# Performance work log

Measured on AMD Instinct MI355X. Metric: run time of the kernel, lower is better.

Reference implementation:

```python
import jax, jax.numpy as jnp
import numpy as np

EMBED_DIM = 1024
NUM_HEADS = 16
HEAD_DIM = EMBED_DIM // NUM_HEADS
BATCH = 2
SEQ = 2048


def setup_inputs() -> dict:
    key = jax.random.key(0)
    ks = jax.random.split(key, 7)
    bound = 1.0 / np.sqrt(EMBED_DIM)  # nn.Linear default init range
    x = jax.random.normal(ks[0], (BATCH, SEQ, EMBED_DIM), dtype=jnp.float32)
    attn_mask = jnp.ones((BATCH, SEQ), dtype=jnp.int32)
    Wq = jax.random.uniform(ks[1], (EMBED_DIM, EMBED_DIM), jnp.float32, -bound, bound)
    bq = jax.random.uniform(ks[2], (EMBED_DIM,), jnp.float32, -bound, bound)
    Wk = jax.random.uniform(ks[3], (EMBED_DIM, EMBED_DIM), jnp.float32, -bound, bound)
    bk = jax.random.uniform(ks[4], (EMBED_DIM,), jnp.float32, -bound, bound)
    Wv = jax.random.uniform(ks[5], (EMBED_DIM, EMBED_DIM), jnp.float32, -bound, bound)
    bv = jax.random.uniform(ks[6], (EMBED_DIM,), jnp.float32, -bound, bound)
    return {"x": x, "attn_mask": attn_mask, "inv_scale": 8,
            "Wq": Wq, "bq": bq, "Wk": Wk, "bk": bk, "Wv": Wv, "bv": bv}


def reference(x, attn_mask, inv_scale, Wq, bq, Wk, bk, Wv, bv):
    bs, seq_len, _ = x.shape
    # Linear layers (torch: y = x @ W.T + b; here W stored as [in,out])
    def split_heads(y):
        return y.reshape(bs, seq_len, NUM_HEADS, HEAD_DIM).transpose(0, 2, 1, 3)  # [b,h,s,d]
    q = split_heads(x @ Wq + bq)
    k = split_heads(x @ Wk + bk)
    v = split_heads(x @ Wv + bv)
    scores = jnp.einsum('bhqd,bhkd->bhqk', q, k) / jnp.asarray(inv_scale, x.dtype)
    mask = (attn_mask == 0)[:, None, None, :]  # True where masked
    scores = jnp.where(mask, -jnp.inf, scores)
    attn = jax.nn.softmax(scores, axis=-1)
    out = jnp.einsum('bhqk,bhkd->bhqd', attn, v)  # [b,h,s,d]
    return out
```

## Files before the change

### kernel.cpp

```cpp
#include <hip/hip_runtime.h>
#include <stdint.h>

typedef __bf16 bf16x8 __attribute__((ext_vector_type(8)));
typedef float f32x4 __attribute__((ext_vector_type(4)));
typedef uint32_t u32x2 __attribute__((ext_vector_type(2)));
typedef uint32_t u32x4 __attribute__((ext_vector_type(4)));

#define MFMA16(a, b, c) __builtin_amdgcn_mfma_f32_16x16x32_bf16((a), (b), (c), 0, 0, 0)

#if __has_builtin(__builtin_amdgcn_exp2f)
#define EXP2F(x) __builtin_amdgcn_exp2f(x)
#else
#define EXP2F(x) exp2f(x)
#endif

__device__ __forceinline__ void gload16(const void* gsrc, void* ldst) {
  __builtin_amdgcn_global_load_lds((__attribute__((address_space(1))) void*)gsrc,
                                   (__attribute__((address_space(3))) void*)ldst, 16, 0, 0);
}

__device__ __forceinline__ uint32_t pkbf(float a, float b) {
  uint16_t ua = __builtin_bit_cast(uint16_t, (__bf16)a);
  uint16_t ub = __builtin_bit_cast(uint16_t, (__bf16)b);
  return (uint32_t)ua | ((uint32_t)ub << 16);
}

__global__ __launch_bounds__(256) void prep_kernel(
    const float* __restrict__ x, const float* __restrict__ Wq,
    const float* __restrict__ Wk, const float* __restrict__ Wv,
    ushort* __restrict__ xb, ushort* __restrict__ wt) {
  int tid = blockIdx.x * 256 + threadIdx.x;
  if (tid < 524288) {
    const f32x4* xp = (const f32x4*)x;
    f32x4 a = xp[tid * 2], b = xp[tid * 2 + 1];
    u32x4 o;
    o[0] = pkbf(a[0], a[1]);
    o[1] = pkbf(a[2], a[3]);
    o[2] = pkbf(b[0], b[1]);
    o[3] = pkbf(b[2], b[3]);
    *(u32x4*)(xb + (size_t)tid * 8) = o;
  } else {
    int r = tid - 524288;
    int mtx = r >> 17;
    int q = r & 131071;
    int n = q & 1023, kc = q >> 10;
    const float* W = (mtx == 0) ? Wq : (mtx == 1) ? Wk : Wv;
    const float* src = W + (size_t)kc * 8 * 1024 + n;
    float v0 = src[0], v1 = src[1024], v2 = src[2048], v3 = src[3072];
    float v4 = src[4096], v5 = src[5120], v6 = src[6144], v7 = src[7168];
    u32x4 o;
    o[0] = pkbf(v0, v1);
    o[1] = pkbf(v2, v3);
    o[2] = pkbf(v4, v5);
    o[3] = pkbf(v6, v7);
    *(u32x4*)(wt + (size_t)mtx * 1048576 + (size_t)n * 1024 + kc * 8) = o;
  }
}

__global__ __launch_bounds__(256, 2) void gemm_qkv(
    const ushort* __restrict__ xb, const ushort* __restrict__ wt,
    const float* __restrict__ bq, const float* __restrict__ bk,
    const float* __restrict__ bv, ushort* __restrict__ Qb,
    ushort* __restrict__ Kb, ushort* __restrict__ Vt) {
  __shared__ ushort ash[2][128 * 64];
  __shared__ ushort bsh[2][128 * 64];
  const int tid = threadIdx.x;
  const int w = tid >> 6, l = tid & 63;
  const int lq = l & 15, g = l >> 4;
  const int z = blockIdx.z;
  const int m0 = blockIdx.x * 128, n0 = blockIdx.y * 128;
  const ushort* A = xb;
  const ushort* B = wt + (size_t)z * 1048576;
  const float* bias = (z == 0) ? bq : (z == 1) ? bk : bv;

  const int lr = l >> 3;
  const int scol = ((l & 7) * 8) ^ (lr * 8);
  const int wr = w >> 1, wc = w & 1;
  const int swz = (lq & 7) << 4;

  f32x4 acc[4][4] = {};

  auto stage = [&](int nb, int t) {
    int k0 = t * 64;
#pragma unroll
    for (int i = 0; i < 4; ++i) {
      int row = w * 32 + i * 8;
      gload16(A + (size_t)(m0 + row + lr) * 1024 + k0 + scol, &ash[nb][row * 64]);
    }
#pragma unroll
    for (int i = 0; i < 4; ++i) {
      int row = w * 32 + i * 8;
      gload16(B + (size_t)(n0 + row + lr) * 1024 + k0 + scol, &bsh[nb][row * 64]);
    }
  };

  stage(0, 0);
  __syncthreads();
  int buf = 0;
  for (int t = 0; t < 16; ++t) {
    if (t < 15) stage(buf ^ 1, t + 1);
    bf16x8 af[4][2], bfr[4][2];
#pragma unroll
    for (int mi = 0; mi < 4; ++mi)
#pragma unroll
      for (int kk = 0; kk < 2; ++kk) {
        int row = wr * 64 + mi * 16 + lq;
        af[mi][kk] = *(const bf16x8*)((const char*)&ash[buf][0] + row * 128 +
                                      ((kk * 64 + g * 16) ^ swz));
      }
#pragma unroll
    for (int ni = 0; ni < 4; ++ni)
#pragma unroll
      for (int kk = 0; kk < 2; ++kk) {
        int row = wc * 64 + ni * 16 + lq;
        bfr[ni][kk] = *(const bf16x8*)((const char*)&bsh[buf][0] + row * 128 +
                                       ((kk * 64 + g * 16) ^ swz));
      }
#pragma unroll
    for (int mi = 0; mi < 4; ++mi)
#pragma unroll
      for (int ni = 0; ni < 4; ++ni) {
        acc[mi][ni] = MFMA16(af[mi][0], bfr[ni][0], acc[mi][ni]);
        acc[mi][ni] = MFMA16(af[mi][1], bfr[ni][1], acc[mi][ni]);
      }
    __syncthreads();
    buf ^= 1;
  }

#pragma unroll
  for (int ni = 0; ni < 4; ++ni) {
    int nn = n0 + wc * 64 + ni * 16 + lq;
    int h = nn >> 6, d = nn & 63;
    float bb = bias[nn];
#pragma unroll
    for (int mi = 0; mi < 4; ++mi) {
      int mbase = m0 + wr * 64 + mi * 16 + g * 4;
      if (z < 2) {
        ushort* dst = (z == 0) ? Qb : Kb;
#pragma unroll
        for (int j = 0; j < 4; ++j) {
          int mm = mbase + j;
          int b = mm >> 11, s = mm & 2047;
          float v = acc[mi][ni][j] + bb;
          dst[((size_t)(b * 16 + h) * 2048 + s) * 64 + d] =
              __builtin_bit_cast(uint16_t, (__bf16)v);
        }
      } else {
        int b = mbase >> 11, s0 = mbase & 2047;
        u32x2 pk;
        pk[0] = pkbf(acc[mi][ni][0] + bb, acc[mi][ni][1] + bb);
        pk[1] = pkbf(acc[mi][ni][2] + bb, acc[mi][ni][3] + bb);
        *(u32x2*)(Vt + ((size_t)(b * 16 + h) * 64 + d) * 2048 + s0) = pk;
      }
    }
  }
}

__global__ __launch_bounds__(256, 2) void attn_kernel(
    const ushort* __restrict__ Qb, const ushort* __restrict__ Kb,
    const ushort* __restrict__ Vt, const int* __restrict__ mask,
    const int* __restrict__ invp, float* __restrict__ out) {
  __shared__ ushort ksh[2][64 * 64];
  __shared__ ushort vsh[2][64 * 64];
  __shared__ ushort psh[4][32 * 64];
  const int tid = threadIdx.x;
  const int w = tid >> 6, l = tid & 63;
  const int lq = l & 15, g = l >> 4;
  const int qt = blockIdx.x, h = blockIdx.y, b = blockIdx.z;
  const int bh = b * 16 + h;
  const ushort* Qp = Qb + ((size_t)bh * 2048 + qt * 128 + w * 32) * 64;
  const ushort* Kp = Kb + (size_t)bh * 2048 * 64;
  const ushort* Vp = Vt + (size_t)bh * 64 * 2048;
  const int* mp = mask + b * 2048;
  const float c = 1.44269504088896341f / (float)(*invp);

  const int lr = l >> 3;
  const int scol = ((l & 7) * 8) ^ (lr * 8);
  const int swz = (lq & 7) << 4;

  bf16x8 qf_[2][2];
#pragma unroll
  for (int qf = 0; qf < 2; ++qf)
#pragma unroll
    for (int kk = 0; kk < 2; ++kk)
      qf_[qf][kk] = *(const bf16x8*)(Qp + (qf * 16 + lq) * 64 + kk * 32 + g * 8);

  f32x4 acco[4][2] = {};
  float m_[2] = {-__builtin_inff(), -__builtin_inff()};
  float l_[2] = {0.f, 0.f};

  auto stage = [&](int nb, int t) {
#pragma unroll
    for (int i = 0; i < 2; ++i) {
      int row = w * 16 + i * 8;
      gload16(Kp + (size_t)(t * 64 + row + lr) * 64 + scol, &ksh[nb][row * 64]);
      gload16(Vp + (size_t)(row + lr) * 2048 + t * 64 + scol, &vsh[nb][row * 64]);
    }
  };
  stage(0, 0);
  __syncthreads();
  int buf = 0;
  for (int t = 0; t < 32; ++t) {
    if (t < 31) stage(buf ^ 1, t + 1);
    f32x4 sc[2][4];
    bf16x8 kf_[4][2];
#pragma unroll
    for (int kf = 0; kf < 4; ++kf)
#pragma unroll
      for (int kk = 0; kk < 2; ++kk) {
        int row = kf * 16 + lq;
        kf_[kf][kk] = *(const bf16x8*)((const char*)&ksh[buf][0] + row * 128 +
                                       ((kk * 64 + g * 16) ^ swz));
      }
#pragma unroll
    for (int qf = 0; qf < 2; ++qf)
#pragma unroll
      for (int kf = 0; kf < 4; ++kf) {
        f32x4 zz = {0.f, 0.f, 0.f, 0.f};
        zz = MFMA16(kf_[kf][0], qf_[qf][0], zz);
        sc[qf][kf] = MFMA16(kf_[kf][1], qf_[qf][1], zz);
      }
    int4 mv[4];
#pragma unroll
    for (int kf = 0; kf < 4; ++kf)
      mv[kf] = *(const int4*)(mp + t * 64 + kf * 16 + g * 4);
#pragma unroll
    for (int qf = 0; qf < 2; ++qf) {
      float mx = -__builtin_inff();
#pragma unroll
      for (int kf = 0; kf < 4; ++kf) {
        sc[qf][kf] *= c;
#pragma unroll
        for (int j = 0; j < 4; ++j) mx = fmaxf(mx, sc[qf][kf][j]);
      }
      mx = fmaxf(mx, __shfl_xor(mx, 16, 64));
      mx = fmaxf(mx, __shfl_xor(mx, 32, 64));
      float mnew = fmaxf(m_[qf], mx);
      float alpha = EXP2F(m_[qf] - mnew);
      m_[qf] = mnew;
      float ps = 0.f;
      int p = qf * 16 + lq;
      char* pbase = (char*)&psh[w][0] + p * 128;
#pragma unroll
      for (int kf = 0; kf < 4; ++kf) {
        float pv[4];
#pragma unroll
        for (int j = 0; j < 4; ++j) {
          float e = EXP2F(sc[qf][kf][j] - mnew);
          int mm = (j == 0) ? mv[kf].x : (j == 1) ? mv[kf].y : (j == 2) ? mv[kf].z : mv[kf].w;
          e = mm ? e : 0.f;
          pv[j] = e;
          ps += e;
        }
        u32x2 pk2;
        pk2[0] = pkbf(pv[0], pv[1]);
        pk2[1] = pkbf(pv[2], pv[3]);
        *(u32x2*)(pbase + ((kf * 32 + g * 8) ^ swz)) = pk2;
      }
      ps += __shfl_xor(ps, 16, 64);
      ps += __shfl_xor(ps, 32, 64);
      l_[qf] = l_[qf] * alpha + ps;
#pragma unroll
      for (int nd = 0; nd < 4; ++nd) acco[nd][qf] *= alpha;
    }
    bf16x8 pf[2][2], vf[4][2];
#pragma unroll
    for (int qf = 0; qf < 2; ++qf)
#pragma unroll
      for (int kc = 0; kc < 2; ++kc) {
        int p = qf * 16 + lq;
        pf[qf][kc] = *(const bf16x8*)((const char*)&psh[w][0] + p * 128 +
                                      ((kc * 64 + g * 16) ^ swz));
      }
#pragma unroll
    for (int nd = 0; nd < 4; ++nd)
#pragma unroll
      for (int kc = 0; kc < 2; ++kc) {
        int row = nd * 16 + lq;
        vf[nd][kc] = *(const bf16x8*)((const char*)&vsh[buf][0] + row * 128 +
                                      ((kc * 64 + g * 16) ^ swz));
      }
#pragma unroll
    for (int nd = 0; nd < 4; ++nd)
#pragma unroll
      for (int qf = 0; qf < 2; ++qf) {
        acco[nd][qf] = MFMA16(vf[nd][0], pf[qf][0], acco[nd][qf]);
        acco[nd][qf] = MFMA16(vf[nd][1], pf[qf][1], acco[nd][qf]);
      }
    __syncthreads();
    buf ^= 1;
  }
#pragma unroll
  for (int qf = 0; qf < 2; ++qf) {
    float r = 1.0f / l_[qf];
    int qrow = qt * 128 + w * 32 + qf * 16 + lq;
#pragma unroll
    for (int nd = 0; nd < 4; ++nd) {
      f32x4 v = acco[nd][qf] * r;
      int d0 = nd * 16 + g * 4;
      *(f32x4*)(out + ((size_t)bh * 2048 + qrow) * 64 + d0) = v;
    }
  }
}

extern "C" void kernel_launch(void* const* d_in, const int* in_sizes, int n_in,
                              void* d_out, int out_size, void* d_ws,
                              size_t ws_size, hipStream_t stream) {
  (void)in_sizes; (void)n_in; (void)out_size; (void)ws_size;
  const float* x = (const float*)d_in[0];
  const int* mask = (const int*)d_in[1];
  const int* invp = (const int*)d_in[2];
  const float* Wq = (const float*)d_in[3];
  const float* bq = (const float*)d_in[4];
  const float* Wk = (const float*)d_in[5];
  const float* bk = (const float*)d_in[6];
  const float* Wv = (const float*)d_in[7];
  const float* bv = (const float*)d_in[8];

  ushort* xb = (ushort*)d_ws;
  ushort* wt = xb + 4194304;
  ushort* Qb = wt + 3145728;
  ushort* Kb = Qb + 4194304;
  ushort* Vt = Kb + 4194304;
  float* out = (float*)d_out;

  prep_kernel<<<3584, 256, 0, stream>>>(x, Wq, Wk, Wv, xb, wt);
  gemm_qkv<<<dim3(32, 8, 3), 256, 0, stream>>>(xb, wt, bq, bk, bv, Qb, Kb, Vt);
  attn_kernel<<<dim3(16, 16, 2), 256, 0, stream>>>(Qb, Kb, Vt, mask, invp, out);
}
```

Baseline: 208.4 us.

## Shrink attention query tile, fold scale into Q, add lazy rescale and XCD block remap

The attention kernel now handles 64 query rows per block (16 per wave) instead of 128, which doubles the grid and raises the launch-bound occupancy to 4. The softmax scale is folded into Q in the QKV GEMM epilogue, and the online-softmax rescale is skipped when the new max exceeds the old one by at most 8 in log2 units. MFMA sections are wrapped in setprio, and both grids are flattened with a remap that spreads blocks across XCDs. Smaller query tiles double K/V reloads per query, and the lazy rescale allows larger exp values before renormalising.

```diff
diff --git a/kernel.cpp b/kernel.cpp
--- a/kernel.cpp
+++ b/kernel.cpp
@@ -60,18 +60,24 @@
 __global__ __launch_bounds__(256, 2) void gemm_qkv(
     const ushort* __restrict__ xb, const ushort* __restrict__ wt,
     const float* __restrict__ bq, const float* __restrict__ bk,
-    const float* __restrict__ bv, ushort* __restrict__ Qb,
-    ushort* __restrict__ Kb, ushort* __restrict__ Vt) {
+    const float* __restrict__ bv, const int* __restrict__ invp,
+    ushort* __restrict__ Qb, ushort* __restrict__ Kb, ushort* __restrict__ Vt) {
   __shared__ ushort ash[2][128 * 64];
   __shared__ ushort bsh[2][128 * 64];
   const int tid = threadIdx.x;
   const int w = tid >> 6, l = tid & 63;
   const int lq = l & 15, g = l >> 4;
-  const int z = blockIdx.z;
-  const int m0 = blockIdx.x * 128, n0 = blockIdx.y * 128;
+
+  const int f = blockIdx.x;
+  const int nf = (f & 7) * 96 + (f >> 3);
+  const int bx = nf / 24, byy = nf % 24;
+  const int z = byy >> 3;
+  const int m0 = bx * 128, n0 = (byy & 7) * 128;
+
   const ushort* A = xb;
   const ushort* B = wt + (size_t)z * 1048576;
   const float* bias = (z == 0) ? bq : (z == 1) ? bk : bv;
+  const float qs = 1.44269504088896341f / (float)(invp[0]);
 
   const int lr = l >> 3;
   const int scol = ((l & 7) * 8) ^ (lr * 8);
@@ -142,6 +148,7 @@
           int mm = mbase + j;
           int b = mm >> 11, s = mm & 2047;
           float v = acc[mi][ni][j] + bb;
+          if (z == 0) v *= qs;
           dst[((size_t)(b * 16 + h) * 2048 + s) * 64 + d] =
               __builtin_bit_cast(uint16_t, (__bf16)v);
         }
@@ -156,38 +163,39 @@
   }
 }
 
-__global__ __launch_bounds__(256, 2) void attn_kernel(
+__global__ __launch_bounds__(256, 4) void attn_kernel(
     const ushort* __restrict__ Qb, const ushort* __restrict__ Kb,
     const ushort* __restrict__ Vt, const int* __restrict__ mask,
-    const int* __restrict__ invp, float* __restrict__ out) {
+    float* __restrict__ out) {
   __shared__ ushort ksh[2][64 * 64];
   __shared__ ushort vsh[2][64 * 64];
-  __shared__ ushort psh[4][32 * 64];
+  __shared__ ushort psh[4][16 * 64];
   const int tid = threadIdx.x;
   const int w = tid >> 6, l = tid & 63;
   const int lq = l & 15, g = l >> 4;
-  const int qt = blockIdx.x, h = blockIdx.y, b = blockIdx.z;
-  const int bh = b * 16 + h;
-  const ushort* Qp = Qb + ((size_t)bh * 2048 + qt * 128 + w * 32) * 64;
+
+  const int f = blockIdx.x;
+  const int nf = ((f & 7) << 7) + (f >> 3);
+  const int qt = nf & 31, bh = nf >> 5;
+  const int b = bh >> 4;
+
+  const ushort* Qp = Qb + ((size_t)bh * 2048 + qt * 64 + w * 16) * 64;
   const ushort* Kp = Kb + (size_t)bh * 2048 * 64;
   const ushort* Vp = Vt + (size_t)bh * 64 * 2048;
   const int* mp = mask + b * 2048;
-  const float c = 1.44269504088896341f / (float)(*invp);
 
   const int lr = l >> 3;
   const int scol = ((l & 7) * 8) ^ (lr * 8);
   const int swz = (lq & 7) << 4;
 
-  bf16x8 qf_[2][2];
-#pragma unroll
-  for (int qf = 0; qf < 2; ++qf)
-#pragma unroll
-    for (int kk = 0; kk < 2; ++kk)
-      qf_[qf][kk] = *(const bf16x8*)(Qp + (qf * 16 + lq) * 64 + kk * 32 + g * 8);
-
-  f32x4 acco[4][2] = {};
-  float m_[2] = {-__builtin_inff(), -__builtin_inff()};
-  float l_[2] = {0.f, 0.f};
+  bf16x8 qf_[2];
+#pragma unroll
+  for (int kk = 0; kk < 2; ++kk)
+    qf_[kk] = *(const bf16x8*)(Qp + lq * 64 + kk * 32 + g * 8);
+
+  f32x4 acco[4] = {};
+  float m_ = -__builtin_inff();
+  float l_ = 0.f;
 
   auto stage = [&](int nb, int t) {
 #pragma unroll
@@ -202,7 +210,6 @@
   int buf = 0;
   for (int t = 0; t < 32; ++t) {
     if (t < 31) stage(buf ^ 1, t + 1);
-    f32x4 sc[2][4];
     bf16x8 kf_[4][2];
 #pragma unroll
     for (int kf = 0; kf < 4; ++kf)
@@ -212,66 +219,60 @@
         kf_[kf][kk] = *(const bf16x8*)((const char*)&ksh[buf][0] + row * 128 +
                                        ((kk * 64 + g * 16) ^ swz));
       }
-#pragma unroll
-    for (int qf = 0; qf < 2; ++qf)
-#pragma unroll
-      for (int kf = 0; kf < 4; ++kf) {
-        f32x4 zz = {0.f, 0.f, 0.f, 0.f};
-        zz = MFMA16(kf_[kf][0], qf_[qf][0], zz);
-        sc[qf][kf] = MFMA16(kf_[kf][1], qf_[qf][1], zz);
-      }
+    f32x4 sc[4];
+    __builtin_amdgcn_s_setprio(1);
+#pragma unroll
+    for (int kf = 0; kf < 4; ++kf) {
+      f32x4 zz = {0.f, 0.f, 0.f, 0.f};
+      zz = MFMA16(kf_[kf][0], qf_[0], zz);
+      sc[kf] = MFMA16(kf_[kf][1], qf_[1], zz);
+    }
+    __builtin_amdgcn_s_setprio(0);
     int4 mv[4];
 #pragma unroll
     for (int kf = 0; kf < 4; ++kf)
       mv[kf] = *(const int4*)(mp + t * 64 + kf * 16 + g * 4);
-#pragma unroll
-    for (int qf = 0; qf < 2; ++qf) {
-      float mx = -__builtin_inff();
-#pragma unroll
-      for (int kf = 0; kf < 4; ++kf) {
-        sc[qf][kf] *= c;
-#pragma unroll
-        for (int j = 0; j < 4; ++j) mx = fmaxf(mx, sc[qf][kf][j]);
-      }
-      mx = fmaxf(mx, __shfl_xor(mx, 16, 64));
-      mx = fmaxf(mx, __shfl_xor(mx, 32, 64));
-      float mnew = fmaxf(m_[qf], mx);
-      float alpha = EXP2F(m_[qf] - mnew);
-      m_[qf] = mnew;
-      float ps = 0.f;
-      int p = qf * 16 + lq;
-      char* pbase = (char*)&psh[w][0] + p * 128;
-#pragma unroll
-      for (int kf = 0; kf < 4; ++kf) {
-        float pv[4];
-#pragma unroll
-        for (int j = 0; j < 4; ++j) {
-          float e = EXP2F(sc[qf][kf][j] - mnew);
-          int mm = (j == 0) ? mv[kf].x : (j == 1) ? mv[kf].y : (j == 2) ? mv[kf].z : mv[kf].w;
-          e = mm ? e : 0.f;
-          pv[j] = e;
-          ps += e;
-        }
-        u32x2 pk2;
-        pk2[0] = pkbf(pv[0], pv[1]);
-        pk2[1] = pkbf(pv[2], pv[3]);
-        *(u32x2*)(pbase + ((kf * 32 + g * 8) ^ swz)) = pk2;
-      }
-      ps += __shfl_xor(ps, 16, 64);
-      ps += __shfl_xor(ps, 32, 64);
-      l_[qf] = l_[qf] * alpha + ps;
-#pragma unroll
-      for (int nd = 0; nd < 4; ++nd) acco[nd][qf] *= alpha;
-    }
-    bf16x8 pf[2][2], vf[4][2];
-#pragma unroll
-    for (int qf = 0; qf < 2; ++qf)
-#pragma unroll
-      for (int kc = 0; kc < 2; ++kc) {
-        int p = qf * 16 + lq;
-        pf[qf][kc] = *(const bf16x8*)((const char*)&psh[w][0] + p * 128 +
-                                      ((kc * 64 + g * 16) ^ swz));
-      }
+    float mx = -__builtin_inff();
+#pragma unroll
+    for (int kf = 0; kf < 4; ++kf)
+#pragma unroll
+      for (int j = 0; j < 4; ++j) mx = fmaxf(mx, sc[kf][j]);
+    mx = fmaxf(mx, __shfl_xor(mx, 16, 64));
+    mx = fmaxf(mx, __shfl_xor(mx, 32, 64));
+    if (!__all(mx - m_ <= 8.f)) {
+      float mnew = fmaxf(m_, mx);
+      float alpha = EXP2F(m_ - mnew);
+      m_ = mnew;
+      l_ *= alpha;
+#pragma unroll
+      for (int nd = 0; nd < 4; ++nd) acco[nd] *= alpha;
+    }
+    float ps = 0.f;
+    char* pbase = (char*)&psh[w][0] + lq * 128;
+#pragma unroll
+    for (int kf = 0; kf < 4; ++kf) {
+      float pv[4];
+#pragma unroll
+      for (int j = 0; j < 4; ++j) {
+        float e = EXP2F(sc[kf][j] - m_);
+        int mm = (j == 0) ? mv[kf].x : (j == 1) ? mv[kf].y : (j == 2) ? mv[kf].z : mv[kf].w;
+        e = mm ? e : 0.f;
+        pv[j] = e;
+        ps += e;
+      }
+      u32x2 pk2;
+      pk2[0] = pkbf(pv[0], pv[1]);
+      pk2[1] = pkbf(pv[2], pv[3]);
+      *(u32x2*)(pbase + ((kf * 32 + g * 8) ^ swz)) = pk2;
+    }
+    ps += __shfl_xor(ps, 16, 64);
+    ps += __shfl_xor(ps, 32, 64);
+    l_ += ps;
+    bf16x8 pf[2], vf[4][2];
+#pragma unroll
+    for (int kc = 0; kc < 2; ++kc)
+      pf[kc] = *(const bf16x8*)((const char*)&psh[w][0] + lq * 128 +
+                                ((kc * 64 + g * 16) ^ swz));
 #pragma unroll
     for (int nd = 0; nd < 4; ++nd)
 #pragma unroll
@@ -280,26 +281,23 @@
         vf[nd][kc] = *(const bf16x8*)((const char*)&vsh[buf][0] + row * 128 +
                                       ((kc * 64 + g * 16) ^ swz));
       }
-#pragma unroll
-    for (int nd = 0; nd < 4; ++nd)
-#pragma unroll
-      for (int qf = 0; qf < 2; ++qf) {
-        acco[nd][qf] = MFMA16(vf[nd][0], pf[qf][0], acco[nd][qf]);
-        acco[nd][qf] = MFMA16(vf[nd][1], pf[qf][1], acco[nd][qf]);
-      }
+    __builtin_amdgcn_s_setprio(1);
+#pragma unroll
+    for (int nd = 0; nd < 4; ++nd) {
+      acco[nd] = MFMA16(vf[nd][0], pf[0], acco[nd]);
+      acco[nd] = MFMA16(vf[nd][1], pf[1], acco[nd]);
+    }
+    __builtin_amdgcn_s_setprio(0);
     __syncthreads();
     buf ^= 1;
   }
-#pragma unroll
-  for (int qf = 0; qf < 2; ++qf) {
-    float r = 1.0f / l_[qf];
-    int qrow = qt * 128 + w * 32 + qf * 16 + lq;
-#pragma unroll
-    for (int nd = 0; nd < 4; ++nd) {
-      f32x4 v = acco[nd][qf] * r;
-      int d0 = nd * 16 + g * 4;
-      *(f32x4*)(out + ((size_t)bh * 2048 + qrow) * 64 + d0) = v;
-    }
+  float r = 1.0f / l_;
+  int qrow = qt * 64 + w * 16 + lq;
+#pragma unroll
+  for (int nd = 0; nd < 4; ++nd) {
+    f32x4 v = acco[nd] * r;
+    int d0 = nd * 16 + g * 4;
+    *(f32x4*)(out + ((size_t)bh * 2048 + qrow) * 64 + d0) = v;
   }
 }
 
@@ -325,6 +323,6 @@
   float* out = (float*)d_out;
 
   prep_kernel<<<3584, 256, 0, stream>>>(x, Wq, Wk, Wv, xb, wt);
-  gemm_qkv<<<dim3(32, 8, 3), 256, 0, stream>>>(xb, wt, bq, bk, bv, Qb, Kb, Vt);
-  attn_kernel<<<dim3(16, 16, 2), 256, 0, stream>>>(Qb, Kb, Vt, mask, invp, out);
-}
+  gemm_qkv<<<768, 256, 0, stream>>>(xb, wt, bq, bk, bv, invp, Qb, Kb, Vt);
+  attn_kernel<<<1024, 256, 0, stream>>>(Qb, Kb, Vt, mask, out);
+}
```

Result: faster. 199.3 us (median of 2 runs) (-4.4%).
